# Optimization experiments

Measured on AMD Instinct MI355X. Metric: run time of the kernel, lower is better.

The kernel has to match this reference:

```python
import jax, jax.numpy as jnp
import numpy as np

BITS = 4
GROUP_SIZE = 128
IN_FEATURES = 4096
OUT_FEATURES = 14336
M = 256  # rows of x; >= kernel_switch_threshold so torch takes the dequant+matmul path


def setup_inputs() -> dict:
    key = jax.random.key(0)
    k1, k2, k3, k4 = jax.random.split(key, 4)
    x = jax.random.normal(k1, (M, IN_FEATURES), dtype=jnp.float16)
    # packed int4 weights: in_features//32*bits rows of int32
    qweight = jax.random.randint(
        k2, (IN_FEATURES // 32 * BITS, OUT_FEATURES), 0, 2**31 - 1, dtype=jnp.int32
    )
    n_groups = IN_FEATURES // GROUP_SIZE
    scales = jax.random.uniform(k3, (n_groups, OUT_FEATURES), dtype=jnp.float32) * 0.01 + 0.001
    # note: module stores zeros as scale*zero product (see pack()); any float works
    zeros = jax.random.uniform(k4, (n_groups, OUT_FEATURES), dtype=jnp.float32) * 0.05
    return {"x": x, "qweight": qweight, "scales": scales, "zeros": zeros}


def reference(x, qweight, scales, zeros):
    # Unpack 8 int4 values from each int32 (little-endian nibbles), matching
    # torch: (qweight[:,None,:] >> wf) & 0xF with wf = [0,4,...,28].
    shifts = jnp.arange(0, 32, BITS, dtype=jnp.int32)          # [8]
    w = (qweight[:, None, :] >> shifts[None, :, None]) & (2**BITS - 1)  # [K/8, 8, N]
    w = w.reshape(-1, GROUP_SIZE, qweight.shape[1])             # [n_groups, group, N]
    s = scales.astype(jnp.float16)[:, None, :]                  # [n_groups, 1, N]
    z = zeros.astype(jnp.float16)[:, None, :]
    # group-wise asymmetric dequant: scale * q - (scale*zero)
    w = (s * w.astype(jnp.float16) - z).reshape(-1, qweight.shape[1])  # [K, N]
    out = jnp.matmul(x, w)                                      # [M, N] fp16
    return out.astype(x.dtype)
```

## Files before the change

### kernel.cpp

```cpp
#include <hip/hip_runtime.h>
#include <hip/hip_fp16.h>

typedef unsigned int u32;
typedef unsigned short u16;
typedef __attribute__((ext_vector_type(8))) _Float16 f16x8;
typedef __attribute__((ext_vector_type(4))) float f32x4;
typedef __attribute__((ext_vector_type(4))) u32 u32x4;

#define K_DIM 4096
#define N_DIM 14336
#define BM 128
#define BN 64
#define BK 64
#define NT 64
#define NBLK 448
#define LDA 72
#define LDB 72

union H2U { u32 u; __half2 h; };

__device__ __forceinline__ u32 pkrtz(float a, float b) {
  return __builtin_bit_cast(u32, __builtin_amdgcn_cvt_pkrtz(a, b));
}

__device__ __forceinline__ u32 dq2(u32 t, __half2 s2, __half2 c2) {
  H2U x; x.u = 0x58005800u | ((t & 0xFu) << 3) | ((t & 0xF0u) << 15);
  H2U r; r.h = __hfma2(s2, x.h, c2);
  return r.u;
}

__global__ __launch_bounds__(512, 4) void kivi_gemm(
    const float* __restrict__ X,
    const int* __restrict__ QW,
    const float* __restrict__ S,
    const float* __restrict__ Z,
    float* __restrict__ O)
{
  __shared__ __align__(16) u16 As[2][BM][LDA];
  __shared__ __align__(16) u16 Bs[2][BN][LDB];

  const int tid  = threadIdx.x;
  const int lane = tid & 63;
  const int w    = tid >> 6;
  const int ws   = w >> 2;
  const int wl   = w & 3;
  const int stid = tid & 255;

  const int b  = blockIdx.x;
  const int L  = (b & 7) * 56 + (b >> 3);
  const int m0 = (L & 1) * BM;
  const int n0 = (L >> 1) * BN;

  const int ncol  = stid & 63;
  const int k8r0  = stid >> 6;
  const int nglob = n0 + ncol;

  const int wm = wl >> 1, wn = wl & 1;
  const int mb = wm * 64, nb = wn * 32;
  const int fr = lane & 15, fq = lane >> 4;

  f32x4 acc[4][2];
#pragma unroll
  for (int mi = 0; mi < 4; ++mi)
#pragma unroll
    for (int ni = 0; ni < 2; ++ni)
      acc[mi][ni] = (f32x4){0.f, 0.f, 0.f, 0.f};

  u32x4 aPk[4];
  int qa, qb;
  float sv, zv;

  auto loadA = [&](int t) {
#pragma unroll
    for (int p = 0; p < 4; ++p) {
      const int ci  = p * 256 + stid;
      const int row = ci >> 3;
      const int c   = ci & 7;
      const float* src = X + (size_t)(m0 + row) * K_DIM + t * BK + c * 8;
      const f32x4 lo = *(const f32x4*)(src);
      const f32x4 hi = *(const f32x4*)(src + 4);
      aPk[p].x = pkrtz(lo.x, lo.y);
      aPk[p].y = pkrtz(lo.z, lo.w);
      aPk[p].z = pkrtz(hi.x, hi.y);
      aPk[p].w = pkrtz(hi.z, hi.w);
    }
  };
  auto writeA = [&]() {
#pragma unroll
    for (int p = 0; p < 4; ++p) {
      const int ci  = p * 256 + stid;
      const int row = ci >> 3;
      const int c   = ci & 7;
      *(u32x4*)&As[ws][row][c * 8] = aPk[p];
    }
  };
  auto loadB = [&](int t) {
    const int r0 = t * 8 + k8r0;
    qa = QW[(size_t)r0 * N_DIM + nglob];
    qb = QW[(size_t)(r0 + 4) * N_DIM + nglob];
    sv = S[(size_t)(t >> 1) * N_DIM + nglob];
    zv = Z[(size_t)(t >> 1) * N_DIM + nglob];
  };
  auto writeB = [&]() {
    const __half sh = __float2half(sv);
    const __half ch = __float2half(fmaf(-128.f, sv, -zv));
    const __half2 s2 = __halves2half2(sh, sh);
    const __half2 c2 = __halves2half2(ch, ch);
#pragma unroll
    for (int h = 0; h < 2; ++h) {
      const u32 q  = (u32)(h ? qb : qa);
      const int k8 = k8r0 + h * 4;
      u32x4 pk;
      pk.x = dq2(q,       s2, c2);
      pk.y = dq2(q >> 8,  s2, c2);
      pk.z = dq2(q >> 16, s2, c2);
      pk.w = dq2(q >> 24, s2, c2);
      *(u32x4*)&Bs[ws][ncol][k8 * 8] = pk;
    }
  };

  loadA(ws); loadB(ws);
  writeA(); writeB();
  __syncthreads();

  for (int i = 0; i < NT / 2; ++i) {
    const bool pf = (i + 1 < NT / 2);
    if (pf) { loadA(2 * i + 2 + ws); loadB(2 * i + 2 + ws); }

#pragma unroll
    for (int ks = 0; ks < 2; ++ks) {
      f16x8 af[4], bv[2];
#pragma unroll
      for (int mi = 0; mi < 4; ++mi)
        af[mi] = *(const f16x8*)&As[ws][mb + mi * 16 + fr][ks * 32 + fq * 8];
#pragma unroll
      for (int ni = 0; ni < 2; ++ni)
        bv[ni] = *(const f16x8*)&Bs[ws][nb + ni * 16 + fr][ks * 32 + fq * 8];
#pragma unroll
      for (int mi = 0; mi < 4; ++mi)
#pragma unroll
        for (int ni = 0; ni < 2; ++ni)
          acc[mi][ni] = __builtin_amdgcn_mfma_f32_16x16x32_f16(
              af[mi], bv[ni], acc[mi][ni], 0, 0, 0);
    }

    __syncthreads();
    if (pf) { writeA(); writeB(); }
    __syncthreads();
  }

  float (*Lr)[68] = reinterpret_cast<float(*)[68]>(&As[0][0][0]);
  if (ws == 1) {
#pragma unroll
    for (int mi = 0; mi < 4; ++mi)
#pragma unroll
      for (int ni = 0; ni < 2; ++ni)
#pragma unroll
        for (int r = 0; r < 4; ++r)
          Lr[mb + mi * 16 + fq * 4 + r][nb + ni * 16 + fr] = acc[mi][ni][r];
  }
  __syncthreads();
  if (ws == 0) {
#pragma unroll
    for (int mi = 0; mi < 4; ++mi)
#pragma unroll
      for (int ni = 0; ni < 2; ++ni)
#pragma unroll
        for (int r = 0; r < 4; ++r) {
          const int row = mb + mi * 16 + fq * 4 + r;
          const int col = nb + ni * 16 + fr;
          O[(size_t)(m0 + row) * N_DIM + n0 + col] = acc[mi][ni][r] + Lr[row][col];
        }
  }
}

extern "C" void kernel_launch(void* const* d_in, const int* in_sizes, int n_in,
                              void* d_out, int out_size, void* d_ws, size_t ws_size,
                              hipStream_t stream) {
  const float* X  = (const float*)d_in[0];
  const int*   QW = (const int*)d_in[1];
  const float* S  = (const float*)d_in[2];
  const float* Zp = (const float*)d_in[3];
  float* O = (float*)d_out;
  hipLaunchKernelGGL(kivi_gemm, dim3(NBLK), dim3(512), 0, stream, X, QW, S, Zp, O);
}
```

Measured before the change: 65.31 us.

## Dequantize int4 weights in registers straight into MFMA operands, skip LDS B tile

Each wave now loads packed int4 weights for its own MFMA B fragments and dequantizes them in registers with the 0x6400 magic-number trick. This removes the B tile's shared-memory staging and reads. The block tile changes from 128x64 to 64x128, and the A tile gets its own double buffer, which drops one barrier per iteration. A's k-order in LDS is permuted to match the interleaved nibble order of the dequantized B. The cost is that both M-waves repeat the same dequant work, and more registers are needed for weights, scales and zeros.

```diff
diff --git a/kernel.cpp b/kernel.cpp
--- a/kernel.cpp
+++ b/kernel.cpp
@@ -9,24 +9,30 @@
 
 #define K_DIM 4096
 #define N_DIM 14336
-#define BM 128
-#define BN 64
+#define BM 64
+#define BN 128
 #define BK 64
-#define NT 64
+#define NITER 32
 #define NBLK 448
 #define LDA 72
-#define LDB 72
 
-union H2U { u32 u; __half2 h; };
+union U4F8 { u32x4 u; f16x8 v; };
+
+__device__ __forceinline__ f16x8 dq8(u32 q, __half2 s2, __half2 d2, __half2 z2) {
+  U4F8 r;
+  const u32 x0 = ( q        & 0x000F000Fu) | 0x64006400u;
+  const u32 x1 = ((q >> 4)  & 0x000F000Fu) | 0x64006400u;
+  const u32 x2 = ((q >> 8)  & 0x000F000Fu) | 0x64006400u;
+  const u32 x3 = ((q >> 12) & 0x000F000Fu) | 0x64006400u;
+  r.u.x = __builtin_bit_cast(u32, __hsub2(__hfma2(__builtin_bit_cast(__half2, x0), s2, d2), z2));
+  r.u.y = __builtin_bit_cast(u32, __hsub2(__hfma2(__builtin_bit_cast(__half2, x1), s2, d2), z2));
+  r.u.z = __builtin_bit_cast(u32, __hsub2(__hfma2(__builtin_bit_cast(__half2, x2), s2, d2), z2));
+  r.u.w = __builtin_bit_cast(u32, __hsub2(__hfma2(__builtin_bit_cast(__half2, x3), s2, d2), z2));
+  return r.v;
+}
 
 __device__ __forceinline__ u32 pkrtz(float a, float b) {
   return __builtin_bit_cast(u32, __builtin_amdgcn_cvt_pkrtz(a, b));
-}
-
-__device__ __forceinline__ u32 dq2(u32 t, __half2 s2, __half2 c2) {
-  H2U x; x.u = 0x58005800u | ((t & 0xFu) << 3) | ((t & 0xF0u) << 15);
-  H2U r; r.h = __hfma2(s2, x.h, c2);
-  return r.u;
 }
 
 __global__ __launch_bounds__(512, 4) void kivi_gemm(
@@ -36,8 +42,7 @@
     const float* __restrict__ Z,
     float* __restrict__ O)
 {
-  __shared__ __align__(16) u16 As[2][BM][LDA];
-  __shared__ __align__(16) u16 Bs[2][BN][LDB];
+  __shared__ __align__(16) u16 As[2][2][BM][LDA];
 
   const int tid  = threadIdx.x;
   const int lane = tid & 63;
@@ -48,113 +53,115 @@
 
   const int b  = blockIdx.x;
   const int L  = (b & 7) * 56 + (b >> 3);
-  const int m0 = (L & 1) * BM;
-  const int n0 = (L >> 1) * BN;
-
-  const int ncol  = stid & 63;
-  const int k8r0  = stid >> 6;
-  const int nglob = n0 + ncol;
+  const int m0 = (L & 3) * BM;
+  const int n0 = (L >> 2) * BN;
 
   const int wm = wl >> 1, wn = wl & 1;
-  const int mb = wm * 64, nb = wn * 32;
+  const int mb = wm * 32, nb = wn * 64;
   const int fr = lane & 15, fq = lane >> 4;
+  const int cb = n0 + nb + fr;
 
-  f32x4 acc[4][2];
+  const int arow = stid >> 2;
+  const int acol = (stid & 3) * 16;
+
+  f32x4 acc[2][4];
 #pragma unroll
-  for (int mi = 0; mi < 4; ++mi)
+  for (int mi = 0; mi < 2; ++mi)
 #pragma unroll
-    for (int ni = 0; ni < 2; ++ni)
+    for (int ni = 0; ni < 4; ++ni)
       acc[mi][ni] = (f32x4){0.f, 0.f, 0.f, 0.f};
 
-  u32x4 aPk[4];
-  int qa, qb;
-  float sv, zv;
+  f32x4 aReg[4];
+  u32 qReg[2][4];
+  float sv[4], zv[4];
 
-  auto loadA = [&](int t) {
+  auto loadAx = [&](int t) {
+    const float* p = X + (size_t)(m0 + arow) * K_DIM + t * BK + acol;
+    aReg[0] = *(const f32x4*)(p);
+    aReg[1] = *(const f32x4*)(p + 4);
+    aReg[2] = *(const f32x4*)(p + 8);
+    aReg[3] = *(const f32x4*)(p + 12);
+  };
+  auto writeAx = [&](int buf) {
 #pragma unroll
-    for (int p = 0; p < 4; ++p) {
-      const int ci  = p * 256 + stid;
-      const int row = ci >> 3;
-      const int c   = ci & 7;
-      const float* src = X + (size_t)(m0 + row) * K_DIM + t * BK + c * 8;
-      const f32x4 lo = *(const f32x4*)(src);
-      const f32x4 hi = *(const f32x4*)(src + 4);
-      aPk[p].x = pkrtz(lo.x, lo.y);
-      aPk[p].y = pkrtz(lo.z, lo.w);
-      aPk[p].z = pkrtz(hi.x, hi.y);
-      aPk[p].w = pkrtz(hi.z, hi.w);
+    for (int c = 0; c < 2; ++c) {
+      u32x4 pk;
+      pk.x = pkrtz(aReg[c * 2][0], aReg[c * 2 + 1][0]);
+      pk.y = pkrtz(aReg[c * 2][1], aReg[c * 2 + 1][1]);
+      pk.z = pkrtz(aReg[c * 2][2], aReg[c * 2 + 1][2]);
+      pk.w = pkrtz(aReg[c * 2][3], aReg[c * 2 + 1][3]);
+      *(u32x4*)&As[ws][buf][arow][acol + c * 8] = pk;
     }
   };
-  auto writeA = [&]() {
+  auto loadBq = [&](int t, int g) {
+    const size_t rbase = (size_t)(t * 8 + fq) * N_DIM + cb;
 #pragma unroll
-    for (int p = 0; p < 4; ++p) {
-      const int ci  = p * 256 + stid;
-      const int row = ci >> 3;
-      const int c   = ci & 7;
-      *(u32x4*)&As[ws][row][c * 8] = aPk[p];
-    }
-  };
-  auto loadB = [&](int t) {
-    const int r0 = t * 8 + k8r0;
-    qa = QW[(size_t)r0 * N_DIM + nglob];
-    qb = QW[(size_t)(r0 + 4) * N_DIM + nglob];
-    sv = S[(size_t)(t >> 1) * N_DIM + nglob];
-    zv = Z[(size_t)(t >> 1) * N_DIM + nglob];
-  };
-  auto writeB = [&]() {
-    const __half sh = __float2half(sv);
-    const __half ch = __float2half(fmaf(-128.f, sv, -zv));
-    const __half2 s2 = __halves2half2(sh, sh);
-    const __half2 c2 = __halves2half2(ch, ch);
+    for (int ks = 0; ks < 2; ++ks)
 #pragma unroll
-    for (int h = 0; h < 2; ++h) {
-      const u32 q  = (u32)(h ? qb : qa);
-      const int k8 = k8r0 + h * 4;
-      u32x4 pk;
-      pk.x = dq2(q,       s2, c2);
-      pk.y = dq2(q >> 8,  s2, c2);
-      pk.z = dq2(q >> 16, s2, c2);
-      pk.w = dq2(q >> 24, s2, c2);
-      *(u32x4*)&Bs[ws][ncol][k8 * 8] = pk;
+      for (int ni = 0; ni < 4; ++ni)
+        qReg[ks][ni] = *(const u32*)(QW + rbase + (size_t)ks * 4 * N_DIM + ni * 16);
+#pragma unroll
+    for (int ni = 0; ni < 4; ++ni) {
+      sv[ni] = S[(size_t)g * N_DIM + cb + ni * 16];
+      zv[ni] = Z[(size_t)g * N_DIM + cb + ni * 16];
     }
   };
 
-  loadA(ws); loadB(ws);
-  writeA(); writeB();
+  loadAx(ws);
+  loadBq(ws, 0);
+  writeAx(0);
   __syncthreads();
 
-  for (int i = 0; i < NT / 2; ++i) {
-    const bool pf = (i + 1 < NT / 2);
-    if (pf) { loadA(2 * i + 2 + ws); loadB(2 * i + 2 + ws); }
+  const __half hneg1024 = __float2half(-1024.f);
+
+  for (int i = 0; i < NITER; ++i) {
+    const int t   = 2 * i + ws;
+    const int cur = i & 1;
+    const bool pf = (i + 1 < NITER);
+
+    if (pf) loadAx(t + 2);
+
+    __half2 s2[4], d2[4], z2[4];
+#pragma unroll
+    for (int ni = 0; ni < 4; ++ni) {
+      const __half sh = __float2half(sv[ni]);
+      const __half zh = __float2half(zv[ni]);
+      const __half dh = __hmul(sh, hneg1024);
+      s2[ni] = __halves2half2(sh, sh);
+      d2[ni] = __halves2half2(dh, dh);
+      z2[ni] = __halves2half2(zh, zh);
+    }
 
 #pragma unroll
     for (int ks = 0; ks < 2; ++ks) {
-      f16x8 af[4], bv[2];
+      f16x8 af[2], bf[4];
 #pragma unroll
-      for (int mi = 0; mi < 4; ++mi)
-        af[mi] = *(const f16x8*)&As[ws][mb + mi * 16 + fr][ks * 32 + fq * 8];
+      for (int mi = 0; mi < 2; ++mi)
+        af[mi] = *(const f16x8*)&As[ws][cur][mb + mi * 16 + fr][ks * 32 + fq * 8];
 #pragma unroll
-      for (int ni = 0; ni < 2; ++ni)
-        bv[ni] = *(const f16x8*)&Bs[ws][nb + ni * 16 + fr][ks * 32 + fq * 8];
+      for (int ni = 0; ni < 4; ++ni)
+        bf[ni] = dq8(qReg[ks][ni], s2[ni], d2[ni], z2[ni]);
 #pragma unroll
-      for (int mi = 0; mi < 4; ++mi)
+      for (int mi = 0; mi < 2; ++mi)
 #pragma unroll
-        for (int ni = 0; ni < 2; ++ni)
+        for (int ni = 0; ni < 4; ++ni)
           acc[mi][ni] = __builtin_amdgcn_mfma_f32_16x16x32_f16(
-              af[mi], bv[ni], acc[mi][ni], 0, 0, 0);
+              af[mi], bf[ni], acc[mi][ni], 0, 0, 0);
     }
 
-    __syncthreads();
-    if (pf) { writeA(); writeB(); }
+    if (pf) {
+      writeAx(cur ^ 1);
+      loadBq(t + 2, i + 1);
+    }
     __syncthreads();
   }
 
-  float (*Lr)[68] = reinterpret_cast<float(*)[68]>(&As[0][0][0]);
+  float (*Lr)[132] = reinterpret_cast<float(*)[132]>(&As[0][0][0][0]);
   if (ws == 1) {
 #pragma unroll
-    for (int mi = 0; mi < 4; ++mi)
+    for (int mi = 0; mi < 2; ++mi)
 #pragma unroll
-      for (int ni = 0; ni < 2; ++ni)
+      for (int ni = 0; ni < 4; ++ni)
 #pragma unroll
         for (int r = 0; r < 4; ++r)
           Lr[mb + mi * 16 + fq * 4 + r][nb + ni * 16 + fr] = acc[mi][ni][r];
@@ -162,9 +169,9 @@
   __syncthreads();
   if (ws == 0) {
 #pragma unroll
-    for (int mi = 0; mi < 4; ++mi)
+    for (int mi = 0; mi < 2; ++mi)
 #pragma unroll
-      for (int ni = 0; ni < 2; ++ni)
+      for (int ni = 0; ni < 4; ++ni)
 #pragma unroll
         for (int r = 0; r < 4; ++r) {
           const int row = mb + mi * 16 + fq * 4 + r;
```

New measurement: 76.78 us. 1.18x slower.
